# Performance work log

Measured on AMD Instinct MI355X. Metric: run time of the kernel, lower is better.

## Reference

```python
import jax, jax.numpy as jnp
import numpy as np

B, H, E, V = 128, 1024, 1024, 40000
L, S, A = 256, 10, 10
L_S, L_A = 1.0, 1.0  # s_copy_lambda / a_copy_lambda
NEG = -1e24


def setup_inputs():
    key = jax.random.key(0)
    ks = jax.random.split(key, 32)
    n = lambda i, shape: jax.random.normal(ks[i], shape, dtype=jnp.float32)
    p = lambda i, shape: jax.random.normal(ks[i], shape, dtype=jnp.float32) * 0.02
    rnn_in = 3 * E + H  # embed + history ctx (H) + state ctx (E) + action ctx (E)
    return {
        "inp": n(0, (B, 1, E)),
        "hidden": n(1, (1, B, H)),
        "hs_vectors": n(2, (B, L, H)),
        "state_gumbel_prob": jax.random.uniform(ks[3], (B, S, V), dtype=jnp.float32),
        "state_gumbel_embed": n(4, (B, S, E)),
        "action_gumbel_prob": jax.random.uniform(ks[5], (B, A, V), dtype=jnp.float32),
        "action_gumbel_embed": n(6, (B, A, E)),
        "history_lens": jax.random.randint(ks[7], (B,), 1, L + 1),
        "history_word_indices": jax.random.randint(ks[8], (B, L), 0, V),
        # history word mlp-attention
        "Wq_hist": p(9, (H, H)), "bq_hist": jnp.zeros((H,), jnp.float32),
        "Wm_hist": p(10, (H, H)), "v_hist": p(11, (H,)),
        # init_s_attn / init_a_attn (query H, memory E)
        "Wq_s": p(12, (H, H)), "bq_s": jnp.zeros((H,), jnp.float32),
        "Wm_s": p(13, (E, H)), "v_s": p(14, (H,)),
        "Wq_a": p(15, (H, H)), "bq_a": jnp.zeros((H,), jnp.float32),
        "Wm_a": p(16, (E, H)), "v_a": p(17, (H,)),
        # sparse_copy_attn (memory E+1)
        "Wq_sc": p(18, (H, H)), "bq_sc": jnp.zeros((H,), jnp.float32),
        "Wm_sc": p(19, (E + 1, H)), "v_sc": p(20, (H,)),
        # GRU (torch layout: [3H, in], gate order r,z,n)
        "W_ih": p(21, (3 * H, rnn_in)), "W_hh": p(22, (3 * H, H)),
        "b_ih": jnp.zeros((3 * H,), jnp.float32), "b_hh": jnp.zeros((3 * H,), jnp.float32),
        # output projection
        "W_out": p(23, (H, V)), "b_out": jnp.zeros((V,), jnp.float32),
    }


def _mlp_scores(q, mem, Wq, bq, Wm, v):
    # q: [B,1,H], mem: [B,L,M] -> additive-attention logits [B,1,L]
    t = jnp.tanh((q @ Wq + bq) + (mem @ Wm))  # [B,L,H]
    return (t @ v)[:, None, :]


def reference(inp, hidden, hs_vectors, state_gumbel_prob, state_gumbel_embed,
              action_gumbel_prob, action_gumbel_embed, history_lens,
              history_word_indices, Wq_hist, bq_hist, Wm_hist, v_hist,
              Wq_s, bq_s, Wm_s, v_s, Wq_a, bq_a, Wm_a, v_a,
              Wq_sc, bq_sc, Wm_sc, v_sc, W_ih, W_hh, b_ih, b_hh, W_out, b_out):
    q0 = jnp.transpose(hidden, (1, 0, 2))  # [B,1,H]
    # --- history word attention (masked mlp attention) ---
    hist_scores = _mlp_scores(q0, hs_vectors, Wq_hist, bq_hist, Wm_hist, v_hist)
    valid = jnp.arange(L)[None, None, :] < history_lens[:, None, None]
    hist_scores = jnp.where(valid, hist_scores, NEG)
    c_his = jax.nn.softmax(hist_scores, axis=-1) @ hs_vectors  # [B,1,H]
    # --- init_consult over state / action gumbel embeddings ---
    sw = jax.nn.softmax(_mlp_scores(q0, state_gumbel_embed, Wq_s, bq_s, Wm_s, v_s), axis=-1)
    c_state = sw @ state_gumbel_embed  # [B,1,E]
    aw = jax.nn.softmax(_mlp_scores(q0, action_gumbel_embed, Wq_a, bq_a, Wm_a, v_a), axis=-1)
    c_action = aw @ action_gumbel_embed  # [B,1,E]
    x = jnp.concatenate([inp, c_his, c_state, c_action], axis=-1)[:, 0, :]  # [B,3E+H]
    # --- single-step GRU cell (torch semantics, gate order r,z,n) ---
    h0 = hidden[0]
    gi = x @ W_ih.T + b_ih
    gh = h0 @ W_hh.T + b_hh
    ir, iz, inn = jnp.split(gi, 3, axis=-1)
    hr, hz, hn = jnp.split(gh, 3, axis=-1)
    r = jax.nn.sigmoid(ir + hr)
    z = jax.nn.sigmoid(iz + hz)
    nact = jnp.tanh(inn + r * hn)
    h_new = (1.0 - z) * nact + z * h0  # [B,H]
    # --- vocab logits + copy logits, joint softmax ---
    gene_logits = h_new @ W_out + b_out  # [B,V]
    cq = h_new[:, None, :]
    hs_logits = jnp.einsum('bqh,blh->bql', cq, hs_vectors)[:, 0, :]  # dot attn, [B,L]
    s_tag = jnp.zeros((B, S, 1), jnp.float32)
    a_tag = jnp.ones((B, A, 1), jnp.float32)
    st_logits = _mlp_scores(cq, jnp.concatenate([state_gumbel_embed, s_tag], -1), Wq_sc, bq_sc, Wm_sc, v_sc)[:, 0, :]
    ac_logits = _mlp_scores(cq, jnp.concatenate([action_gumbel_embed, a_tag], -1), Wq_sc, bq_sc, Wm_sc, v_sc)[:, 0, :]
    all_logits = jnp.concatenate([gene_logits, hs_logits, st_logits, ac_logits], axis=-1)
    wp = jax.nn.softmax(all_logits, axis=-1)  # [B, V+L+S+A]
    gene_p = wp[:, :V]
    hs_w = wp[:, V:V + L]
    st_w = wp[:, V + L:V + L + S]
    ac_w = wp[:, V + L + S:]
    # --- copy-distribution mixing ---
    scp = jnp.einsum('bs,bsv->bv', st_w, state_gumbel_prob)
    acp = jnp.einsum('ba,bav->bv', ac_w, action_gumbel_prob)
    gene_p = gene_p + L_S * scp + L_A * acp
    copy_p = jnp.zeros((B, V), jnp.float32).at[jnp.arange(B)[:, None], history_word_indices].add(hs_w)
    out = jnp.log(gene_p + copy_p)[:, None, :]  # [B,1,V]
    return out, h_new[None]
```

## Files before the change

### kernel.cpp

```cpp
#include <hip/hip_runtime.h>
#include <stdint.h>

typedef __attribute__((ext_vector_type(4))) float f32x4;
typedef __attribute__((ext_vector_type(2))) unsigned int u32x2;
typedef __attribute__((ext_vector_type(4))) unsigned int u32x4;
typedef __attribute__((ext_vector_type(8))) short bf16x8;

#define BV (128*40000)

__device__ __forceinline__ unsigned rne_bf16(float f) {
    unsigned x = __float_as_uint(f);
    return ((x + 0x7FFFu + ((x >> 16) & 1u)) >> 16) & 0xFFFFu;
}
__device__ __forceinline__ unsigned pack2(float a, float b) {
    return rne_bf16(a) | (rne_bf16(b) << 16);
}
__device__ __forceinline__ float bf2f(unsigned u) {
    return __uint_as_float((u & 0xFFFFu) << 16);
}
__device__ __forceinline__ float sigm(float x) { return 1.0f / (1.0f + expf(-x)); }
__device__ __forceinline__ float ftanh(float x) {
    float e = __expf(2.0f * x);
    return 1.0f - 2.0f / (e + 1.0f);
}

__device__ __forceinline__ void gload16(const void* g, void* l) {
    __builtin_amdgcn_global_load_lds(
        (const __attribute__((address_space(1))) unsigned*)g,
        (__attribute__((address_space(3))) unsigned*)l, 16, 0, 0);
}

struct BigArgs {
    const unsigned short *hs, *WmhT, *se, *ae, *WmsT, *WmaT, *WmscT;
    const float *qh_h, *bq_h, *v_h;
    const float *qh_s, *bq_s, *v_s;
    const float *qh_a, *bq_a, *v_a;
    float *hsc, *stsc, *acsc;
    unsigned short *mseh, *maeh;
};

__global__ __launch_bounds__(512, 1) void k_big(
    BigArgs a, int* __restrict__ ctr, const int* __restrict__ prefix,
    const int* __restrict__ ntp) {
    __shared__ unsigned short As[2][16384];
    __shared__ unsigned short Bs[2][16384];
    __shared__ int sTile;
    __shared__ int rows_tab[256];

    const int nTiles = ntp[0], Mp = ntp[1];
    const int t = threadIdx.x, lane = t & 63, wv = t >> 6;
    const int l16 = lane & 15, lq = lane >> 4;
    const int wm = wv >> 2, wn = wv & 3;
    const int srowL = t >> 3;
    const int gccA = ((t & 7) ^ (srowL & 7)) << 3;
    const int swz = l16 & 7;
    const int c0 = ((lq ^ swz) << 3);
    const int A0 = (wm << 13) + (l16 << 6);
    const int B0 = ((wn >> 1) << 13) + ((((wn & 1) << 6) + l16) << 6);

#define STQA(ktt, d, q) gload16(gAr[q] + (ktt) * 64, &As[d][((q) << 12) + (wv << 9)])
#define STQB(ktt, d, q) gload16(gB + ((size_t)(q) << 16) + (ktt) * 64, &Bs[d][((q) << 12) + (wv << 9)])

    for (;;) {
        __syncthreads();
        if (t == 0) sTile = atomicAdd(ctr, 1);
        __syncthreads();
        const int wg = sTile;
        if (wg >= nTiles) return;

        const unsigned short *Abase, *Bt;
        const float *rb = nullptr, *cb = nullptr, *vv = nullptr;
        float* out = nullptr;
        unsigned short* outh = nullptr;
        int m0, n0, vrows, cls;
        if (wg < 40) {
            cls = 0;
            int op = wg / 20, r = wg - op * 20;
            int mt = r >> 2, nt2 = r & 3;
            if (op == 0) { Abase = a.se; Bt = a.WmsT; rb = a.qh_s; cb = a.bq_s; vv = a.v_s; out = a.stsc; }
            else         { Abase = a.ae; Bt = a.WmaT; rb = a.qh_a; cb = a.bq_a; vv = a.v_a; out = a.acsc; }
            m0 = mt << 8; n0 = nt2 << 8; vrows = 256;
        } else if (wg < 80) {
            cls = 1;
            int r = wg - 40;
            int op = r / 20; r -= op * 20;
            int mt = r >> 2, nt2 = r & 3;
            Abase = op ? a.ae : a.se; Bt = a.WmscT;
            outh = op ? a.maeh : a.mseh;
            m0 = mt << 8; n0 = nt2 << 8; vrows = 256;
        } else {
            cls = 2;
            int h = wg - 80;
            int m = h >> 2, n = h & 3;
            Abase = a.hs; Bt = a.WmhT; rb = a.qh_h; cb = a.bq_h; vv = a.v_h; out = a.hsc;
            m0 = m << 8; n0 = n << 8;
            vrows = Mp - m0; if (vrows > 256) vrows = 256;
        }

        if (t < 256) {
            int rid;
            if (cls != 2) {
                rid = m0 + t;
            } else {
                int g = m0 + t;
                if (g < Mp) {
                    int lo = 0, hi = 128;
                    while (hi - lo > 1) {
                        int mid = (lo + hi) >> 1;
                        if (prefix[mid] <= g) lo = mid; else hi = mid;
                    }
                    rid = (lo << 8) + (g - prefix[lo]);
                } else {
                    rid = 0;
                }
            }
            rows_tab[t] = rid;
        }
        __syncthreads();

        const unsigned short* gAr[4];
#pragma unroll
        for (int q = 0; q < 4; ++q)
            gAr[q] = Abase + ((size_t)rows_tab[srowL + (q << 6)] << 10) + gccA;
        const unsigned short* gB = Bt + (size_t)(n0 + srowL) * 1024 + gccA;

        f32x4 acc[8][4];
#pragma unroll
        for (int i = 0; i < 8; ++i)
#pragma unroll
            for (int j = 0; j < 4; ++j) acc[i][j] = (f32x4){0.f, 0.f, 0.f, 0.f};

        STQA(0, 0, 0); STQA(0, 0, 2);
        STQB(0, 0, 0); STQB(0, 0, 1); STQB(0, 0, 2); STQB(0, 0, 3);
        STQA(0, 0, 1); STQA(0, 0, 3);
        __builtin_amdgcn_sched_barrier(0);
        asm volatile("s_waitcnt vmcnt(2)" ::: "memory");
        __builtin_amdgcn_s_barrier();
        __builtin_amdgcn_sched_barrier(0);

        for (int kt = 0; kt < 16; ++kt) {
            const int cur = kt & 1, dn = cur ^ 1, kn = kt + 1;
            const bool pre = kt < 15;
            const unsigned short* ab = As[cur];
            const unsigned short* bb = Bs[cur];
            bf16x8 bk0[4], bk1[4], af[4];
            if (pre) { STQA(kn, dn, 0); STQA(kn, dn, 2); }
#pragma unroll
            for (int nf = 0; nf < 4; ++nf) bk0[nf] = *(const bf16x8*)(bb + B0 + (nf << 10) + c0);
#pragma unroll
            for (int mf = 0; mf < 4; ++mf) af[mf] = *(const bf16x8*)(ab + A0 + (mf << 10) + c0);
            __builtin_amdgcn_s_setprio(1);
#pragma unroll
            for (int mf = 0; mf < 4; ++mf)
#pragma unroll
                for (int nf = 0; nf < 4; ++nf)
                    acc[mf][nf] = __builtin_amdgcn_mfma_f32_16x16x32_bf16(af[mf], bk0[nf], acc[mf][nf], 0, 0, 0);
            __builtin_amdgcn_s_setprio(0);
            if (pre) { STQB(kn, dn, 0); STQB(kn, dn, 1); }
#pragma unroll
            for (int nf = 0; nf < 4; ++nf) bk1[nf] = *(const bf16x8*)(bb + B0 + (nf << 10) + (c0 ^ 32));
#pragma unroll
            for (int mf = 0; mf < 4; ++mf) af[mf] = *(const bf16x8*)(ab + A0 + (mf << 10) + (c0 ^ 32));
            __builtin_amdgcn_s_setprio(1);
#pragma unroll
            for (int mf = 0; mf < 4; ++mf)
#pragma unroll
                for (int nf = 0; nf < 4; ++nf)
                    acc[mf][nf] = __builtin_amdgcn_mfma_f32_16x16x32_bf16(af[mf], bk1[nf], acc[mf][nf], 0, 0, 0);
            __builtin_amdgcn_s_setprio(0);
            if (pre) { STQB(kn, dn, 2); STQB(kn, dn, 3); }
            __builtin_amdgcn_sched_barrier(0);
            if (pre) asm volatile("s_waitcnt vmcnt(6)" ::: "memory");
            else     asm volatile("s_waitcnt vmcnt(0)" ::: "memory");
            __builtin_amdgcn_s_barrier();
            __builtin_amdgcn_sched_barrier(0);
#pragma unroll
            for (int mf = 0; mf < 4; ++mf) af[mf] = *(const bf16x8*)(ab + A0 + ((4 + mf) << 10) + c0);
            __builtin_amdgcn_s_setprio(1);
#pragma unroll
            for (int mf = 0; mf < 4; ++mf)
#pragma unroll
                for (int nf = 0; nf < 4; ++nf)
                    acc[4 + mf][nf] = __builtin_amdgcn_mfma_f32_16x16x32_bf16(af[mf], bk0[nf], acc[4 + mf][nf], 0, 0, 0);
            __builtin_amdgcn_s_setprio(0);
            if (pre) { STQA(kn, dn, 1); STQA(kn, dn, 3); }
#pragma unroll
            for (int mf = 0; mf < 4; ++mf) af[mf] = *(const bf16x8*)(ab + A0 + ((4 + mf) << 10) + (c0 ^ 32));
            __builtin_amdgcn_s_setprio(1);
#pragma unroll
            for (int mf = 0; mf < 4; ++mf)
#pragma unroll
                for (int nf = 0; nf < 4; ++nf)
                    acc[4 + mf][nf] = __builtin_amdgcn_mfma_f32_16x16x32_bf16(af[mf], bk1[nf], acc[4 + mf][nf], 0, 0, 0);
            __builtin_amdgcn_s_setprio(0);
            __builtin_amdgcn_sched_barrier(0);
            if (pre) asm volatile("s_waitcnt vmcnt(2)" ::: "memory");
            else     asm volatile("s_waitcnt vmcnt(0)" ::: "memory");
            __builtin_amdgcn_s_barrier();
            __builtin_amdgcn_sched_barrier(0);
        }

        if (cls == 1) {
            int gcs4[4];
#pragma unroll
            for (int nf = 0; nf < 4; ++nf) gcs4[nf] = n0 + (wn << 6) + (nf << 4) + l16;
#pragma unroll
            for (int mf = 0; mf < 8; ++mf) {
#pragma unroll
                for (int r = 0; r < 4; ++r) {
                    int grow = m0 + (wm << 7) + (mf << 4) + (lq << 2) + r;
#pragma unroll
                    for (int nf = 0; nf < 4; ++nf)
                        outh[(size_t)grow * 1024 + gcs4[nf]] = (unsigned short)rne_bf16(acc[mf][nf][r]);
                }
            }
        } else {
            float cbv[4], vvv[4];
            int gcs[4];
#pragma unroll
            for (int nf = 0; nf < 4; ++nf) {
                int gc = n0 + (wn << 6) + (nf << 4) + l16;
                gcs[nf] = gc; cbv[nf] = cb[gc]; vvv[nf] = vv[gc];
            }
#pragma unroll
            for (int mf = 0; mf < 8; ++mf) {
                int rloc = (wm << 7) + (mf << 4);
                if (rloc < vrows) {
#pragma unroll
                    for (int r = 0; r < 4; ++r) {
                        int lrow = rloc + (lq << 2) + r;
                        if (lrow >= vrows) continue;
                        int gr = m0 + lrow;
                        int bidx = (cls == 2) ? (rows_tab[lrow] >> 8) : (gr / 10);
                        const float* rbp = rb + ((size_t)bidx << 10);
                        float s = 0.f;
#pragma unroll
                        for (int nf = 0; nf < 4; ++nf) {
                            float x = acc[mf][nf][r] + rbp[gcs[nf]] + cbv[nf];
                            s += ftanh(x) * vvv[nf];
                        }
#pragma unroll
                        for (int m2 = 1; m2 < 16; m2 <<= 1) s += __shfl_xor(s, m2, 64);
                        if (l16 == 0) atomicAdd(&out[gr], s);
                    }
                }
            }
        }
    }
#undef STQA
#undef STQB
}

__device__ __forceinline__ void mgemm2(
    const unsigned short* __restrict__ A, const unsigned short* __restrict__ Bt,
    float* __restrict__ out,
    int m0, int n0, int kb, int ke, int ldk, int ldc)
{
    __shared__ unsigned short As[2][4096];
    __shared__ unsigned short Bs[2][4096];
    const int t = threadIdx.x, lane = t & 63, wv = t >> 6;
    const int l16 = lane & 15, lq = lane >> 4;
    const int wm = wv >> 1, wn = wv & 1;

    const int srow = lane >> 2, scol = (lane & 3) << 3;
    const unsigned short* gA0 = A + (size_t)(m0 + (wv << 4) + srow) * ldk + kb + scol;
    const unsigned short* gA1 = gA0 + (size_t)64 * ldk;
    const unsigned short* gB0 = Bt + (size_t)(n0 + (wv << 4) + srow) * ldk + kb + scol;
    const unsigned short* gB1 = gB0 + (size_t)64 * ldk;
    unsigned short* lA0 = &As[0][wv << 9];
    unsigned short* lA1 = &As[0][(wv + 4) << 9];
    unsigned short* lB0 = &Bs[0][wv << 9];
    unsigned short* lB1 = &Bs[0][(wv + 4) << 9];

    f32x4 acc[4][4];
#pragma unroll
    for (int i = 0; i < 4; ++i)
#pragma unroll
        for (int j = 0; j < 4; ++j) acc[i][j] = (f32x4){0.f, 0.f, 0.f, 0.f};

    const int NS = (ke - kb) >> 5;
    gload16(gA0, lA0); gload16(gA1, lA1);
    gload16(gB0, lB0); gload16(gB1, lB1);

    for (int s = 0; s < NS; ++s) {
        __syncthreads();
        if (s + 1 < NS) {
            const int nb = (s + 1) & 1, ko = (s + 1) << 5;
            gload16(gA0 + ko, lA0 + (nb << 12)); gload16(gA1 + ko, lA1 + (nb << 12));
            gload16(gB0 + ko, lB0 + (nb << 12)); gload16(gB1 + ko, lB1 + (nb << 12));
        }
        const unsigned short* ab = As[s & 1];
        const unsigned short* bb = Bs[s & 1];
        bf16x8 af[4], bfv[4];
#pragma unroll
        for (int i = 0; i < 4; ++i)
            af[i] = *(const bf16x8*)(ab + (((wm << 6) + (i << 4) + l16) << 5) + (lq << 3));
#pragma unroll
        for (int i = 0; i < 4; ++i)
            bfv[i] = *(const bf16x8*)(bb + (((wn << 6) + (i << 4) + l16) << 5) + (lq << 3));
#pragma unroll
        for (int mf = 0; mf < 4; ++mf)
#pragma unroll
            for (int nf = 0; nf < 4; ++nf)
                acc[mf][nf] = __builtin_amdgcn_mfma_f32_16x16x32_bf16(af[mf], bfv[nf], acc[mf][nf], 0, 0, 0);
    }

#pragma unroll
    for (int mf = 0; mf < 4; ++mf) {
        int gr0 = m0 + (wm << 6) + (mf << 4) + (lq << 2);
#pragma unroll
        for (int nf = 0; nf < 4; ++nf) {
            int gc = n0 + (wn << 6) + (nf << 4) + l16;
#pragma unroll
            for (int r = 0; r < 4; ++r)
                atomicAdd(&out[(size_t)(gr0 + r) * ldc + gc], acc[mf][nf][r]);
        }
    }
}

__device__ __forceinline__ void gene_body(
    const unsigned short* __restrict__ hnb, const float* __restrict__ Wout,
    const float* __restrict__ b_out, float* __restrict__ out, int n0)
{
    __shared__ unsigned short As[2][4096];
    __shared__ unsigned short Bs[2][4096];
    const int t = threadIdx.x, lane = t & 63, wv = t >> 6;
    const int l16 = lane & 15, lq = lane >> 4;
    const int wm = wv >> 1, wn = wv & 1;

    const int srow = lane >> 2, scol = (lane & 3) << 3;
    const unsigned short* gA0 = hnb + (size_t)((wv << 4) + srow) * 1024 + scol;
    const unsigned short* gA1 = gA0 + (size_t)64 * 1024;
    unsigned short* lA0 = &As[0][wv << 9];
    unsigned short* lA1 = &As[0][(wv + 4) << 9];

    const int bn = t & 127, kh = t >> 7;
    const bool ok = (n0 + bn) < 40000;
    const float* gB = Wout + (size_t)(kh * 16) * 40000 + (n0 + bn);

    f32x4 acc[4][4];
#pragma unroll
    for (int i = 0; i < 4; ++i)
#pragma unroll
        for (int j = 0; j < 4; ++j) acc[i][j] = (f32x4){0.f, 0.f, 0.f, 0.f};

    auto stageB = [&](int buf, int ko) {
        const float* src = gB + (size_t)ko * 40000;
        float f[16];
#pragma unroll
        for (int j = 0; j < 16; ++j) f[j] = ok ? src[(size_t)j * 40000] : 0.0f;
        u32x4* d = (u32x4*)&Bs[buf][bn * 32 + kh * 16];
        d[0] = (u32x4){pack2(f[0],f[1]), pack2(f[2],f[3]), pack2(f[4],f[5]), pack2(f[6],f[7])};
        d[1] = (u32x4){pack2(f[8],f[9]), pack2(f[10],f[11]), pack2(f[12],f[13]), pack2(f[14],f[15])};
    };

    gload16(gA0, lA0); gload16(gA1, lA1); stageB(0, 0);
    for (int s = 0; s < 32; ++s) {
        __syncthreads();
        if (s + 1 < 32) {
            const int nb = (s + 1) & 1, ko = (s + 1) << 5;
            gload16(gA0 + ko, lA0 + (nb << 12)); gload16(gA1 + ko, lA1 + (nb << 12));
            stageB(nb, ko);
        }
        const unsigned short* ab = As[s & 1];
        const unsigned short* bb = Bs[s & 1];
        bf16x8 af[4], bfv[4];
#pragma unroll
        for (int i = 0; i < 4; ++i)
            af[i] = *(const bf16x8*)(ab + (((wm << 6) + (i << 4) + l16) << 5) + (lq << 3));
#pragma unroll
        for (int i = 0; i < 4; ++i)
            bfv[i] = *(const bf16x8*)(bb + (((wn << 6) + (i << 4) + l16) << 5) + (lq << 3));
#pragma unroll
        for (int mf = 0; mf < 4; ++mf)
#pragma unroll
            for (int nf = 0; nf < 4; ++nf)
                acc[mf][nf] = __builtin_amdgcn_mfma_f32_16x16x32_bf16(af[mf], bfv[nf], acc[mf][nf], 0, 0, 0);
    }
#pragma unroll
    for (int mf = 0; mf < 4; ++mf) {
        int gr0 = (wm << 6) + (mf << 4) + (lq << 2);
#pragma unroll
        for (int nf = 0; nf < 4; ++nf) {
            int gc = n0 + (wn << 6) + (nf << 4) + l16;
            if (gc < 40000) {
                float bo = b_out[gc];
#pragma unroll
                for (int r = 0; r < 4; ++r)
                    out[(size_t)(gr0 + r) * 40000 + gc] = acc[mf][nf][r] + bo;
            }
        }
    }
}

__global__ __launch_bounds__(256) void k_qh4(
    const unsigned short* q0, const unsigned short* W0, const unsigned short* W1,
    const unsigned short* W2, float* o0, float* o1, float* o2) {
    const unsigned short* W = W0; float* o = o0;
    if (blockIdx.z == 1) { W = W1; o = o1; }
    if (blockIdx.z == 2) { W = W2; o = o2; }
    int kb = blockIdx.y << 8;
    mgemm2(q0, W, o, 0, blockIdx.x * 128, kb, kb + 256, 1024, 1024);
}

__global__ __launch_bounds__(256) void k_gigh2(
    const unsigned short* xb, const unsigned short* q0,
    const unsigned short* Wih, const unsigned short* Whh, float* gi, float* gh) {
    if (blockIdx.z == 0) {
        int kb = blockIdx.y << 9;
        mgemm2(xb, Wih, gi, 0, blockIdx.x * 128, kb, kb + 512, 4096, 3072);
    } else {
        if (blockIdx.y >= 2) return;
        int kb = blockIdx.y << 9;
        mgemm2(q0, Whh, gh, 0, blockIdx.x * 128, kb, kb + 512, 1024, 3072);
    }
}

__global__ __launch_bounds__(256) void k_geneR(
    const unsigned short* __restrict__ hnb, const float* __restrict__ Wout,
    const float* __restrict__ b_out, float* __restrict__ out,
    const float* __restrict__ sprob, const float* __restrict__ aprob,
    const float* __restrict__ wtil, float* __restrict__ R) {
    int id = blockIdx.x;
    if (id < 313) {
        gene_body(hnb, Wout, b_out, out, id << 7);
        return;
    }
    int rid = id - 313;
    int b = rid / 40, ch = rid - b * 40;
    int t = threadIdx.x;
    __shared__ float wsb[20];
    if (t < 20) wsb[t] = wtil[b * 20 + t];
    __syncthreads();
    if (t >= 250) return;
    int v4 = ch * 250 + t;
    size_t base = (size_t)b * 10000 + v4;
    f32x4 r = {0.f, 0.f, 0.f, 0.f};
#pragma unroll
    for (int s = 0; s < 10; ++s) {
        f32x4 pv = ((const f32x4*)sprob)[((size_t)b * 10 + s) * 10000 + v4];
        f32x4 av = ((const f32x4*)aprob)[((size_t)b * 10 + s) * 10000 + v4];
        float ws = wsb[s], wa = wsb[10 + s];
#pragma unroll
        for (int j = 0; j < 4; ++j) r[j] += ws * pv[j] + wa * av[j];
    }
    ((f32x4*)R)[base] = r;
}

struct PrepArgs {
    const float* cs[6]; unsigned short* cd[6]; int pre[7];
    const float* ts[8]; unsigned short* td[8];
    const int* lens; int* prefix; int* nt;
};
__global__ __launch_bounds__(256) void k_prep(PrepArgs a) {
    int bid = blockIdx.x, t = threadIdx.x;
    if (bid < 2048) {
        __shared__ float tile[64][65];
        int z = bid >> 8, rem = bid & 255, y = rem >> 4, x = rem & 15;
        const float* in = a.ts[z];
        unsigned short* ot = a.td[z];
        int k0 = y << 6, n0 = x << 6;
        int tr = t >> 6, tc = t & 63;
#pragma unroll
        for (int i = 0; i < 16; ++i) {
            int r = (i << 2) + tr;
            tile[r][tc] = in[(size_t)(k0 + r) * 1024 + n0 + tc];
        }
        __syncthreads();
#pragma unroll
        for (int i = 0; i < 16; ++i) {
            int r = (i << 2) + tr;
            ot[(size_t)(n0 + r) * 1024 + k0 + tc] = (unsigned short)rne_bf16(tile[tc][r]);
        }
    } else if (bid == 2048) {
        __shared__ int sc[128];
        if (t < 128) sc[t] = a.lens[t];
        __syncthreads();
        for (int off = 1; off < 128; off <<= 1) {
            int x = (t >= off && t < 128) ? sc[t - off] : 0;
            __syncthreads();
            if (t < 128) sc[t] += x;
            __syncthreads();
        }
        if (t == 0) a.prefix[0] = 0;
        if (t < 128) a.prefix[t + 1] = sc[t];
        if (t == 127) {
            int Mp = sc[127];
            a.nt[0] = 80 + (((Mp + 255) >> 8) << 2);
            a.nt[1] = Mp;
        }
    } else {
        int total = a.pre[6];
        for (int i = (bid - 2049) * 256 + t; i < total; i += 2048 * 256) {
            int seg = 0;
            while (i >= a.pre[seg + 1]) ++seg;
            int loc = i - a.pre[seg];
            const f32x4* s4 = (const f32x4*)a.cs[seg] + (size_t)loc * 2;
            f32x4 q0 = s4[0], q1 = s4[1];
            ((u32x4*)a.cd[seg])[loc] =
                (u32x4){pack2(q0[0],q0[1]), pack2(q0[2],q0[3]), pack2(q1[0],q1[1]), pack2(q1[2],q1[3])};
        }
    }
}

__device__ __forceinline__ void softmax10(const float* src, float* dst) {
    float m = src[0];
    for (int i = 1; i < 10; ++i) m = fmaxf(m, src[i]);
    float z = 0.f, e[10];
    for (int i = 0; i < 10; ++i) { e[i] = expf(src[i] - m); z += e[i]; }
    float iz = 1.0f / z;
    for (int i = 0; i < 10; ++i) dst[i] = e[i] * iz;
}

__global__ __launch_bounds__(256) void k_ctx(
    const float* __restrict__ scores, const int* __restrict__ lens,
    const int* __restrict__ prefix,
    const unsigned short* __restrict__ hs,
    const float* __restrict__ inp, const float* __restrict__ st_sc, const float* __restrict__ ac_sc,
    const unsigned short* __restrict__ se, const unsigned short* __restrict__ ae,
    unsigned short* __restrict__ xb) {
    int b = blockIdx.x, t = threadIdx.x;
    __shared__ float w[256];
    __shared__ float red[256];
    __shared__ float sw[10], aw[10];
    int len = lens[b];
    int base = prefix[b];
    bool valid = t < len;
    float s = valid ? scores[base + t] : -3.0e38f;
    red[t] = s;
    __syncthreads();
    for (int st = 128; st > 0; st >>= 1) { if (t < st) red[t] = fmaxf(red[t], red[t + st]); __syncthreads(); }
    float m = red[0];
    __syncthreads();
    float e = valid ? expf(s - m) : 0.0f;
    red[t] = e;
    __syncthreads();
    for (int st = 128; st > 0; st >>= 1) { if (t < st) red[t] += red[t + st]; __syncthreads(); }
    float Z = red[0];
    __syncthreads();
    w[t] = e / Z;
    if (t == 0) softmax10(st_sc + b * 10, sw);
    if (t == 64) softmax10(ac_sc + b * 10, aw);
    f32x4 iv = ((const f32x4*)(inp + (size_t)b * 1024))[t];
    *((u32x2*)(xb + (size_t)b * 4096) + t) = (u32x2){pack2(iv[0], iv[1]), pack2(iv[2], iv[3])};
    __syncthreads();
    float a0 = 0.f, a1 = 0.f, a2 = 0.f, a3 = 0.f;
    for (int l = 0; l < 256; ++l) {
        float wl = w[l];
        if (wl == 0.0f) continue;
        u32x2 u = *((const u32x2*)(hs + ((size_t)b * 256 + l) * 1024) + t);
        a0 += wl * bf2f(u[0]); a1 += wl * bf2f(u[0] >> 16);
        a2 += wl * bf2f(u[1]); a3 += wl * bf2f(u[1] >> 16);
    }
    *((u32x2*)(xb + (size_t)b * 4096 + 1024) + t) = (u32x2){pack2(a0, a1), pack2(a2, a3)};
    float cs0=0,cs1=0,cs2=0,cs3=0, ca0=0,ca1=0,ca2=0,ca3=0;
#pragma unroll
    for (int q = 0; q < 10; ++q) {
        u32x2 us = *((const u32x2*)(se + ((size_t)b * 10 + q) * 1024) + t);
        u32x2 ua = *((const u32x2*)(ae + ((size_t)b * 10 + q) * 1024) + t);
        float ws = sw[q], wa = aw[q];
        cs0 += ws * bf2f(us[0]); cs1 += ws * bf2f(us[0] >> 16);
        cs2 += ws * bf2f(us[1]); cs3 += ws * bf2f(us[1] >> 16);
        ca0 += wa * bf2f(ua[0]); ca1 += wa * bf2f(ua[0] >> 16);
        ca2 += wa * bf2f(ua[1]); ca3 += wa * bf2f(ua[1] >> 16);
    }
    *((u32x2*)(xb + (size_t)b * 4096 + 2048) + t) = (u32x2){pack2(cs0, cs1), pack2(cs2, cs3)};
    *((u32x2*)(xb + (size_t)b * 4096 + 3072) + t) = (u32x2){pack2(ca0, ca1), pack2(ca2, ca3)};
}

__global__ __launch_bounds__(1024) void k_gruhsl(
    const float* __restrict__ gi, const float* __restrict__ gh,
    const float* __restrict__ b_ih, const float* __restrict__ b_hh,
    const float* __restrict__ h0, float* __restrict__ hnew,
    unsigned short* __restrict__ hnb,
    const unsigned short* __restrict__ hs, float* __restrict__ hsl,
    const unsigned short* __restrict__ WqscT, float* __restrict__ qsc) {
    int b = blockIdx.x, y = blockIdx.y, j = threadIdx.x;
    size_t i = (size_t)b * 1024 + j;
    const float* gib = gi + (size_t)b * 3072;
    const float* ghb = gh + (size_t)b * 3072;
    float r = sigm(gib[j] + b_ih[j] + ghb[j] + b_hh[j]);
    float z = sigm(gib[1024 + j] + b_ih[1024 + j] + ghb[1024 + j] + b_hh[1024 + j]);
    float hn = ghb[2048 + j] + b_hh[2048 + j];
    float n = tanhf(gib[2048 + j] + b_ih[2048 + j] + r * hn);
    float h = (1.0f - z) * n + z * h0[i];
    if (y == 0) {
        hnew[i] = h;
        hnb[i] = (unsigned short)rne_bf16(h);
    }
    __shared__ float hsm[1024];
    hsm[j] = h;
    __syncthreads();
    {
        float acn = 0.f;
        const u32x4* wr = (const u32x4*)(WqscT + ((size_t)j << 10));
        int st = y << 6;
#pragma unroll 4
        for (int k8 = st; k8 < st + 64; ++k8) {
            u32x4 u = wr[k8];
            const float* hp = hsm + (k8 << 3);
            acn += hp[0]*bf2f(u[0]) + hp[1]*bf2f(u[0]>>16)
                 + hp[2]*bf2f(u[1]) + hp[3]*bf2f(u[1]>>16)
                 + hp[4]*bf2f(u[2]) + hp[5]*bf2f(u[2]>>16)
                 + hp[6]*bf2f(u[3]) + hp[7]*bf2f(u[3]>>16);
        }
        atomicAdd(&qsc[(size_t)b * 1024 + j], acn);
    }
    int wave = j >> 6, lane = j & 63;
    float hr[16];
#pragma unroll
    for (int k = 0; k < 16; ++k) hr[k] = hsm[lane * 16 + k];
    for (int l = (y << 7) + wave; l < (y << 7) + 128; l += 16) {
        const u32x4* row = (const u32x4*)(hs + ((size_t)b * 256 + l) * 1024);
        u32x4 u0 = row[lane * 2], u1 = row[lane * 2 + 1];
        float s = hr[0]*bf2f(u0[0]) + hr[1]*bf2f(u0[0]>>16) + hr[2]*bf2f(u0[1]) + hr[3]*bf2f(u0[1]>>16)
                + hr[4]*bf2f(u0[2]) + hr[5]*bf2f(u0[2]>>16) + hr[6]*bf2f(u0[3]) + hr[7]*bf2f(u0[3]>>16)
                + hr[8]*bf2f(u1[0]) + hr[9]*bf2f(u1[0]>>16) + hr[10]*bf2f(u1[1]) + hr[11]*bf2f(u1[1]>>16)
                + hr[12]*bf2f(u1[2]) + hr[13]*bf2f(u1[2]>>16) + hr[14]*bf2f(u1[3]) + hr[15]*bf2f(u1[3]>>16);
#pragma unroll
        for (int msk = 1; msk < 64; msk <<= 1) s += __shfl_xor(s, msk, 64);
        if (lane == 0) hsl[b * 256 + l] = s;
    }
}

__global__ __launch_bounds__(256) void k_stacep(
    const unsigned short* __restrict__ mseh, const unsigned short* __restrict__ maeh,
    const float* __restrict__ qsc, const float* __restrict__ bq_sc,
    const float* __restrict__ v_sc, const float* __restrict__ tagrow,
    float* __restrict__ stlg, float* __restrict__ aclg,
    float* __restrict__ mtil, float* __restrict__ wtil) {
    int b = blockIdx.x, t = threadIdx.x, w = t >> 6, lane = t & 63;
    __shared__ float res[20];
    const float* qb = qsc + (size_t)b * 1024;
    for (int r = w; r < 20; r += 4) {
        bool ac = r >= 10;
        int s = ac ? r - 10 : r;
        const unsigned short* mm = (ac ? maeh : mseh) + ((size_t)b * 10 + s) * 1024;
        float acc = 0.f;
#pragma unroll
        for (int j2 = 0; j2 < 16; ++j2) {
            int c = lane + (j2 << 6);
            float x = bf2f(mm[c]) + qb[c] + bq_sc[c];
            if (ac) x += tagrow[c];
            acc += ftanh(x) * v_sc[c];
        }
#pragma unroll
        for (int m2 = 1; m2 < 64; m2 <<= 1) acc += __shfl_xor(acc, m2, 64);
        if (lane == 0) res[r] = acc;
    }
    __syncthreads();
    if (t < 10) stlg[b * 10 + t] = res[t];
    if (t >= 64 && t < 74) aclg[b * 10 + (t - 64)] = res[10 + (t - 64)];
    if (t == 128) {
        float mt = res[0];
        for (int i2 = 1; i2 < 20; ++i2) mt = fmaxf(mt, res[i2]);
        mtil[b] = mt;
        for (int i2 = 0; i2 < 20; ++i2) wtil[b * 20 + i2] = expf(res[i2] - mt);
    }
}

__global__ __launch_bounds__(256) void k_smsc(
    const float* __restrict__ gene, const float* __restrict__ hsl,
    const float* __restrict__ stl, const float* __restrict__ acl,
    const int* __restrict__ hwi,
    float* __restrict__ mbuf, float* __restrict__ zbuf, float* __restrict__ copyp) {
    int b = blockIdx.x, t = threadIdx.x;
    __shared__ float red[256];
    const f32x4* g4 = (const f32x4*)(gene + (size_t)b * 40000);
    float mx = -3.0e38f;
    for (int i = t; i < 10000; i += 256) {
        f32x4 q = g4[i];
        mx = fmaxf(mx, fmaxf(fmaxf(q[0], q[1]), fmaxf(q[2], q[3])));
    }
    float hv = hsl[b * 256 + t];
    mx = fmaxf(mx, hv);
    if (t < 10) mx = fmaxf(mx, fmaxf(stl[b * 10 + t], acl[b * 10 + t]));
    red[t] = mx; __syncthreads();
    for (int s = 128; s > 0; s >>= 1) { if (t < s) red[t] = fmaxf(red[t], red[t + s]); __syncthreads(); }
    float m = red[0];
    __syncthreads();
    float sum = 0.f;
    for (int i = t; i < 10000; i += 256) {
        f32x4 q = g4[i];
        sum += expf(q[0]-m) + expf(q[1]-m) + expf(q[2]-m) + expf(q[3]-m);
    }
    sum += expf(hv - m);
    if (t < 10) sum += expf(stl[b * 10 + t] - m) + expf(acl[b * 10 + t] - m);
    red[t] = sum; __syncthreads();
    for (int s = 128; s > 0; s >>= 1) { if (t < s) red[t] += red[t + s]; __syncthreads(); }
    float Z = red[0];
    if (t == 0) { mbuf[b] = m; zbuf[b] = Z; }
    float wv = expf(hv - m) / Z;
    atomicAdd(copyp + (size_t)b * 40000 + hwi[b * 256 + t], wv);
}

__global__ __launch_bounds__(256) void k_final(
    float* __restrict__ gene_out, const float* __restrict__ copyp,
    const float* __restrict__ R, const float* __restrict__ mbuf,
    const float* __restrict__ zbuf, const float* __restrict__ mtil) {
    int b = blockIdx.y, t = threadIdx.x;
    int v4 = blockIdx.x * 256 + t;
    if (v4 < 10000) {
        float m = mbuf[b], iz = 1.0f / zbuf[b];
        float sb = expf(mtil[b] - m) * iz;
        size_t base = (size_t)b * 10000 + v4;
        f32x4 g = ((const f32x4*)gene_out)[base];
        f32x4 c = ((const f32x4*)copyp)[base];
        f32x4 rr = ((const f32x4*)R)[base];
        f32x4 r;
#pragma unroll
        for (int j = 0; j < 4; ++j)
            r[j] = logf(expf(g[j] - m) * iz + c[j] + rr[j] * sb);
        ((f32x4*)gene_out)[base] = r;
    }
}

#define OFF_QH_H  0
#define OFF_QH_S  131072
#define OFF_QH_A  262144
#define OFF_QSC   393216
#define OFF_GI    524288
#define OFF_GH    917504
#define OFF_HSC   1310720
#define OFF_STSC  1343488
#define OFF_ACSC  1344768
#define OFF_STLG  1346048
#define OFF_ACLG  1347328
#define OFF_CTR   1348608
#define OFF_PFX   1348736
#define OFF_NT    1348904
#define ZERO_FLOATS 1348936
#define OFF_HSL   1348992
#define OFF_M     1381760
#define OFF_Z     1381888
#define OFF_COPY  1382016
#define OFF_MTIL  6502016
#define OFF_WTIL  6502144
#define FLOAT_TOTAL 6504704
#define SO_HS     0
#define SO_SE     33554432
#define SO_AE     34865152
#define SO_Q0     36175872
#define SO_X      36306944
#define SO_HNB    36831232
#define SO_WQHT   36962304
#define SO_WQST   38010880
#define SO_WQAT   39059456
#define SO_WQSCT  40108032
#define SO_WMHT   41156608
#define SO_WMST   42205184
#define SO_WMAT   43253760
#define SO_WMSCT  44302336
#define SO_WIH    45350912
#define SO_WHH    57933824
#define SO_MSE    61079552
#define SO_MAE    62390272

extern "C" void kernel_launch(void* const* d_in, const int* in_sizes, int n_in,
                              void* d_out, int out_size, void* d_ws, size_t ws_size,
                              hipStream_t stream) {
    const float* inp     = (const float*)d_in[0];
    const float* hidden  = (const float*)d_in[1];
    const float* hs      = (const float*)d_in[2];
    const float* sprob   = (const float*)d_in[3];
    const float* se      = (const float*)d_in[4];
    const float* aprob   = (const float*)d_in[5];
    const float* ae      = (const float*)d_in[6];
    const int*   lens    = (const int*)d_in[7];
    const int*   hwi     = (const int*)d_in[8];
    const float* Wq_hist = (const float*)d_in[9];
    const float* bq_hist = (const float*)d_in[10];
    const float* Wm_hist = (const float*)d_in[11];
    const float* v_hist  = (const float*)d_in[12];
    const float* Wq_s    = (const float*)d_in[13];
    const float* bq_s    = (const float*)d_in[14];
    const float* Wm_s    = (const float*)d_in[15];
    const float* v_s     = (const float*)d_in[16];
    const float* Wq_a    = (const float*)d_in[17];
    const float* bq_a    = (const float*)d_in[18];
    const float* Wm_a    = (const float*)d_in[19];
    const float* v_a     = (const float*)d_in[20];
    const float* Wq_sc   = (const float*)d_in[21];
    const float* bq_sc   = (const float*)d_in[22];
    const float* Wm_sc   = (const float*)d_in[23];
    const float* v_sc    = (const float*)d_in[24];
    const float* W_ih    = (const float*)d_in[25];
    const float* W_hh    = (const float*)d_in[26];
    const float* b_ih    = (const float*)d_in[27];
    const float* b_hh    = (const float*)d_in[28];
    const float* W_out   = (const float*)d_in[29];
    const float* b_out   = (const float*)d_in[30];

    float* out  = (float*)d_out;
    float* w    = (float*)d_ws;
    float* hnew = out + BV;
    unsigned short* sb = (unsigned short*)(w + FLOAT_TOTAL);

    float* qh_h = w + OFF_QH_H;  float* qh_s = w + OFF_QH_S;  float* qh_a = w + OFF_QH_A;
    float* qsc  = w + OFF_QSC;   float* gi   = w + OFF_GI;    float* gh   = w + OFF_GH;
    float* hsc  = w + OFF_HSC;   float* stsc = w + OFF_STSC;  float* acsc = w + OFF_ACSC;
    float* stlg = w + OFF_STLG;  float* aclg = w + OFF_ACLG;
    float* hsl  = w + OFF_HSL;   float* mbuf = w + OFF_M;     float* zbuf = w + OFF_Z;
    float* copyp = w + OFF_COPY;
    float* mtil = w + OFF_MTIL;  float* wtil = w + OFF_WTIL;
    int*   ctr  = (int*)(w + OFF_CTR);
    int*   pfx  = (int*)(w + OFF_PFX);
    int*   ntb  = (int*)(w + OFF_NT);

    unsigned short* hs_bf = sb + SO_HS;   unsigned short* se_bf = sb + SO_SE;
    unsigned short* ae_bf = sb + SO_AE;   unsigned short* q0_bf = sb + SO_Q0;
    unsigned short* x_bf  = sb + SO_X;    unsigned short* hnb   = sb + SO_HNB;
    unsigned short* WqhT  = sb + SO_WQHT; unsigned short* WqsT  = sb + SO_WQST;
    unsigned short* WqaT  = sb + SO_WQAT; unsigned short* WqscT = sb + SO_WQSCT;
    unsigned short* WmhT  = sb + SO_WMHT; unsigned short* WmsT  = sb + SO_WMST;
    unsigned short* WmaT  = sb + SO_WMAT; unsigned short* WmscT = sb + SO_WMSCT;
    unsigned short* WihB  = sb + SO_WIH;  unsigned short* WhhB  = sb + SO_WHH;
    unsigned short* mseh  = sb + SO_MSE;  unsigned short* maeh  = sb + SO_MAE;
    float* Rbuf = (float*)(sb + SO_WIH);

    dim3 blk(256);

    hipMemsetAsync(w, 0, (size_t)ZERO_FLOATS * 4, stream);
    hipMemsetAsync(copyp, 0, (size_t)BV * 4, stream);

    PrepArgs pa;
    pa.cs[0]=hs; pa.cs[1]=se; pa.cs[2]=ae; pa.cs[3]=hidden; pa.cs[4]=W_ih; pa.cs[5]=W_hh;
    pa.cd[0]=hs_bf; pa.cd[1]=se_bf; pa.cd[2]=ae_bf; pa.cd[3]=q0_bf; pa.cd[4]=WihB; pa.cd[5]=WhhB;
    pa.pre[0]=0; pa.pre[1]=4194304; pa.pre[2]=4358144; pa.pre[3]=4521984;
    pa.pre[4]=4538368; pa.pre[5]=6111232; pa.pre[6]=6504448;
    pa.ts[0]=Wq_hist; pa.ts[1]=Wq_s; pa.ts[2]=Wq_a; pa.ts[3]=Wq_sc;
    pa.ts[4]=Wm_hist; pa.ts[5]=Wm_s; pa.ts[6]=Wm_a; pa.ts[7]=Wm_sc;
    pa.td[0]=WqhT; pa.td[1]=WqsT; pa.td[2]=WqaT; pa.td[3]=WqscT;
    pa.td[4]=WmhT; pa.td[5]=WmsT; pa.td[6]=WmaT; pa.td[7]=WmscT;
    pa.lens = lens; pa.prefix = pfx; pa.nt = ntb;
    k_prep<<<dim3(4097), blk, 0, stream>>>(pa);

    k_qh4<<<dim3(8, 4, 3), blk, 0, stream>>>(q0_bf, WqhT, WqsT, WqaT, qh_h, qh_s, qh_a);

    BigArgs ba;
    ba.hs = hs_bf; ba.WmhT = WmhT; ba.se = se_bf; ba.ae = ae_bf;
    ba.WmsT = WmsT; ba.WmaT = WmaT; ba.WmscT = WmscT;
    ba.qh_h = qh_h; ba.bq_h = bq_hist; ba.v_h = v_hist;
    ba.qh_s = qh_s; ba.bq_s = bq_s; ba.v_s = v_s;
    ba.qh_a = qh_a; ba.bq_a = bq_a; ba.v_a = v_a;
    ba.hsc = hsc; ba.stsc = stsc; ba.acsc = acsc;
    ba.mseh = mseh; ba.maeh = maeh;
    k_big<<<dim3(256), dim3(512), 0, stream>>>(ba, ctr, pfx, ntb);

    k_ctx<<<dim3(128), blk, 0, stream>>>(hsc, lens, pfx, hs_bf, inp, stsc, acsc, se_bf, ae_bf, x_bf);
    k_gigh2<<<dim3(24, 8, 2), blk, 0, stream>>>(x_bf, q0_bf, WihB, WhhB, gi, gh);
    k_gruhsl<<<dim3(128, 2), dim3(1024), 0, stream>>>(gi, gh, b_ih, b_hh, hidden, hnew, hnb,
                                                      hs_bf, hsl, WqscT, qsc);
    k_stacep<<<dim3(128), blk, 0, stream>>>(mseh, maeh, qsc, bq_sc, v_sc,
                                            Wm_sc + (size_t)1024 * 1024, stlg, aclg, mtil, wtil);
    k_geneR<<<dim3(313 + 5120), blk, 0, stream>>>(hnb, W_out, b_out, out, sprob, aprob, wtil, Rbuf);
    k_smsc<<<dim3(128), blk, 0, stream>>>(out, hsl, stlg, aclg, hwi, mbuf, zbuf, copyp);
    k_final<<<dim3(40, 128), blk, 0, stream>>>(out, copyp, Rbuf, mbuf, zbuf, mtil);

    (void)in_sizes; (void)n_in; (void)out_size; (void)ws_size;
}
```

Before: 561.6 us.

## Fold query projections, GRU weight conversion and sparse-copy scoring into existing kernels

Moves the three query-projection GEMMs into k_big as its first persistent tiles, with other tiles spin-waiting on a completion counter. The W_ih/W_hh bf16 conversion moves from k_prep into trailing k_big tiles. The k_stacep kernel is folded into k_gruhsl, and k_geneR now computes the exp weights itself. Some sched_barriers in the GEMM loop are also removed. This removes kernel launches and serial gaps, at the cost of a cross-block spin dependency and a single-block-column qsc computation in the GRU kernel.

```diff
diff --git a/kernel.cpp b/kernel.cpp
--- a/kernel.cpp
+++ b/kernel.cpp
@@ -32,22 +32,24 @@
 
 struct BigArgs {
     const unsigned short *hs, *WmhT, *se, *ae, *WmsT, *WmaT, *WmscT;
-    const float *qh_h, *bq_h, *v_h;
-    const float *qh_s, *bq_s, *v_s;
-    const float *qh_a, *bq_a, *v_a;
+    const unsigned short *q0, *Wq0T, *Wq1T, *Wq2T;
+    const float *Wihf, *Whhf;
+    unsigned short *WihB, *WhhB;
+    const float *bq_h, *v_h, *bq_s, *v_s, *bq_a, *v_a;
+    float *qh_h, *qh_s, *qh_a;
     float *hsc, *stsc, *acsc;
     unsigned short *mseh, *maeh;
 };
 
 __global__ __launch_bounds__(512, 1) void k_big(
-    BigArgs a, int* __restrict__ ctr, const int* __restrict__ prefix,
-    const int* __restrict__ ntp) {
+    BigArgs a, int* __restrict__ ctr, int* __restrict__ dqh,
+    const int* __restrict__ prefix, const int* __restrict__ ntp) {
     __shared__ unsigned short As[2][16384];
     __shared__ unsigned short Bs[2][16384];
     __shared__ int sTile;
     __shared__ int rows_tab[256];
 
-    const int nTiles = ntp[0], Mp = ntp[1];
+    const int nTiles = ntp[0], Mp = ntp[1], cvtb = ntp[2];
     const int t = threadIdx.x, lane = t & 63, wv = t >> 6;
     const int l16 = lane & 15, lq = lane >> 4;
     const int wm = wv >> 2, wn = wv & 3;
@@ -68,21 +70,44 @@
         const int wg = sTile;
         if (wg >= nTiles) return;
 
+        if (wg >= cvtb) {
+            const int G_IH = 1572864;
+            int g0 = (wg - cvtb) * 30720 + t;
+#pragma unroll 4
+            for (int it = 0; it < 60; ++it, g0 += 512) {
+                const f32x4* s4;
+                u32x4* d4;
+                if (g0 < G_IH) { s4 = (const f32x4*)a.Wihf + (size_t)g0 * 2; d4 = (u32x4*)a.WihB + g0; }
+                else { int g2 = g0 - G_IH; s4 = (const f32x4*)a.Whhf + (size_t)g2 * 2; d4 = (u32x4*)a.WhhB + g2; }
+                f32x4 q0 = s4[0], q1 = s4[1];
+                *d4 = (u32x4){pack2(q0[0],q0[1]), pack2(q0[2],q0[3]), pack2(q1[0],q1[1]), pack2(q1[2],q1[3])};
+            }
+            continue;
+        }
+
         const unsigned short *Abase, *Bt;
         const float *rb = nullptr, *cb = nullptr, *vv = nullptr;
         float* out = nullptr;
         unsigned short* outh = nullptr;
         int m0, n0, vrows, cls;
-        if (wg < 40) {
+        if (wg < 12) {
+            cls = 4;
+            int op = wg >> 2;
+            Abase = a.q0;
+            Bt = (op == 0) ? a.Wq0T : (op == 1) ? a.Wq1T : a.Wq2T;
+            out = (op == 0) ? a.qh_h : (op == 1) ? a.qh_s : a.qh_a;
+            m0 = 0; n0 = (wg & 3) << 8; vrows = 128;
+        } else if (wg < 52) {
             cls = 0;
-            int op = wg / 20, r = wg - op * 20;
+            int r = wg - 12;
+            int op = r / 20; r -= op * 20;
             int mt = r >> 2, nt2 = r & 3;
             if (op == 0) { Abase = a.se; Bt = a.WmsT; rb = a.qh_s; cb = a.bq_s; vv = a.v_s; out = a.stsc; }
             else         { Abase = a.ae; Bt = a.WmaT; rb = a.qh_a; cb = a.bq_a; vv = a.v_a; out = a.acsc; }
             m0 = mt << 8; n0 = nt2 << 8; vrows = 256;
-        } else if (wg < 80) {
+        } else if (wg < 92) {
             cls = 1;
-            int r = wg - 40;
+            int r = wg - 52;
             int op = r / 20; r -= op * 20;
             int mt = r >> 2, nt2 = r & 3;
             Abase = op ? a.ae : a.se; Bt = a.WmscT;
@@ -90,7 +115,7 @@
             m0 = mt << 8; n0 = nt2 << 8; vrows = 256;
         } else {
             cls = 2;
-            int h = wg - 80;
+            int h = wg - 92;
             int m = h >> 2, n = h & 3;
             Abase = a.hs; Bt = a.WmhT; rb = a.qh_h; cb = a.bq_h; vv = a.v_h; out = a.hsc;
             m0 = m << 8; n0 = n << 8;
@@ -136,7 +161,6 @@
         __builtin_amdgcn_sched_barrier(0);
         asm volatile("s_waitcnt vmcnt(2)" ::: "memory");
         __builtin_amdgcn_s_barrier();
-        __builtin_amdgcn_sched_barrier(0);
 
         for (int kt = 0; kt < 16; ++kt) {
             const int cur = kt & 1, dn = cur ^ 1, kn = kt + 1;
@@ -173,7 +197,6 @@
             if (pre) asm volatile("s_waitcnt vmcnt(6)" ::: "memory");
             else     asm volatile("s_waitcnt vmcnt(0)" ::: "memory");
             __builtin_amdgcn_s_barrier();
-            __builtin_amdgcn_sched_barrier(0);
 #pragma unroll
             for (int mf = 0; mf < 4; ++mf) af[mf] = *(const bf16x8*)(ab + A0 + ((4 + mf) << 10) + c0);
             __builtin_amdgcn_s_setprio(1);
@@ -197,7 +220,6 @@
             if (pre) asm volatile("s_waitcnt vmcnt(2)" ::: "memory");
             else     asm volatile("s_waitcnt vmcnt(0)" ::: "memory");
             __builtin_amdgcn_s_barrier();
-            __builtin_amdgcn_sched_barrier(0);
         }
 
         if (cls == 1) {
@@ -214,7 +236,28 @@
                         outh[(size_t)grow * 1024 + gcs4[nf]] = (unsigned short)rne_bf16(acc[mf][nf][r]);
                 }
             }
+        } else if (cls == 4) {
+#pragma unroll
+            for (int mf = 0; mf < 8; ++mf) {
+                int rloc = (wm << 7) + (mf << 4);
+                if (rloc < vrows) {
+#pragma unroll
+                    for (int r = 0; r < 4; ++r) {
+                        int gr = rloc + (lq << 2) + r;
+#pragma unroll
+                        for (int nf = 0; nf < 4; ++nf) {
+                            int gc = n0 + (wn << 6) + (nf << 4) + l16;
+                            out[(size_t)gr * 1024 + gc] = acc[mf][nf][r];
+                        }
+                    }
+                }
+            }
+            __threadfence();
+            __syncthreads();
+            if (t == 0) atomicAdd(dqh, 1);
         } else {
+            if (t == 0) { while (atomicAdd(dqh, 0) < 12) { } }
+            __syncthreads();
             float cbv[4], vvv[4];
             int gcs[4];
 #pragma unroll
@@ -393,16 +436,6 @@
     }
 }
 
-__global__ __launch_bounds__(256) void k_qh4(
-    const unsigned short* q0, const unsigned short* W0, const unsigned short* W1,
-    const unsigned short* W2, float* o0, float* o1, float* o2) {
-    const unsigned short* W = W0; float* o = o0;
-    if (blockIdx.z == 1) { W = W1; o = o1; }
-    if (blockIdx.z == 2) { W = W2; o = o2; }
-    int kb = blockIdx.y << 8;
-    mgemm2(q0, W, o, 0, blockIdx.x * 128, kb, kb + 256, 1024, 1024);
-}
-
 __global__ __launch_bounds__(256) void k_gigh2(
     const unsigned short* xb, const unsigned short* q0,
     const unsigned short* Wih, const unsigned short* Whh, float* gi, float* gh) {
@@ -420,7 +453,8 @@
     const unsigned short* __restrict__ hnb, const float* __restrict__ Wout,
     const float* __restrict__ b_out, float* __restrict__ out,
     const float* __restrict__ sprob, const float* __restrict__ aprob,
-    const float* __restrict__ wtil, float* __restrict__ R) {
+    const float* __restrict__ stlg, const float* __restrict__ aclg,
+    const float* __restrict__ mtil, float* __restrict__ R) {
     int id = blockIdx.x;
     if (id < 313) {
         gene_body(hnb, Wout, b_out, out, id << 7);
@@ -430,7 +464,8 @@
     int b = rid / 40, ch = rid - b * 40;
     int t = threadIdx.x;
     __shared__ float wsb[20];
-    if (t < 20) wsb[t] = wtil[b * 20 + t];
+    if (t < 10) wsb[t] = expf(stlg[b * 10 + t] - mtil[b]);
+    else if (t < 20) wsb[t] = expf(aclg[b * 10 + (t - 10)] - mtil[b]);
     __syncthreads();
     if (t >= 250) return;
     int v4 = ch * 250 + t;
@@ -448,7 +483,7 @@
 }
 
 struct PrepArgs {
-    const float* cs[6]; unsigned short* cd[6]; int pre[7];
+    const float* cs[4]; unsigned short* cd[4]; int pre[5];
     const float* ts[8]; unsigned short* td[8];
     const int* lens; int* prefix; int* nt;
 };
@@ -486,11 +521,13 @@
         if (t < 128) a.prefix[t + 1] = sc[t];
         if (t == 127) {
             int Mp = sc[127];
-            a.nt[0] = 80 + (((Mp + 255) >> 8) << 2);
+            int H4 = ((Mp + 255) >> 8) << 2;
+            a.nt[0] = 92 + H4 + 64;
             a.nt[1] = Mp;
+            a.nt[2] = 92 + H4;
         }
     } else {
-        int total = a.pre[6];
+        int total = a.pre[4];
         for (int i = (bid - 2049) * 256 + t; i < total; i += 2048 * 256) {
             int seg = 0;
             while (i >= a.pre[seg + 1]) ++seg;
@@ -574,7 +611,11 @@
     const float* __restrict__ h0, float* __restrict__ hnew,
     unsigned short* __restrict__ hnb,
     const unsigned short* __restrict__ hs, float* __restrict__ hsl,
-    const unsigned short* __restrict__ WqscT, float* __restrict__ qsc) {
+    const unsigned short* __restrict__ WqscT,
+    const unsigned short* __restrict__ mseh, const unsigned short* __restrict__ maeh,
+    const float* __restrict__ bq_sc, const float* __restrict__ v_sc,
+    const float* __restrict__ tagrow,
+    float* __restrict__ stlg, float* __restrict__ aclg, float* __restrict__ mtil) {
     int b = blockIdx.x, y = blockIdx.y, j = threadIdx.x;
     size_t i = (size_t)b * 1024 + j;
     const float* gib = gi + (size_t)b * 3072;
@@ -584,19 +625,20 @@
     float hn = ghb[2048 + j] + b_hh[2048 + j];
     float n = tanhf(gib[2048 + j] + b_ih[2048 + j] + r * hn);
     float h = (1.0f - z) * n + z * h0[i];
+    __shared__ float hsm[1024];
+    __shared__ float qs[1024];
+    __shared__ float res[20];
     if (y == 0) {
         hnew[i] = h;
         hnb[i] = (unsigned short)rne_bf16(h);
     }
-    __shared__ float hsm[1024];
     hsm[j] = h;
     __syncthreads();
-    {
+    if (y == 0) {
         float acn = 0.f;
         const u32x4* wr = (const u32x4*)(WqscT + ((size_t)j << 10));
-        int st = y << 6;
 #pragma unroll 4
-        for (int k8 = st; k8 < st + 64; ++k8) {
+        for (int k8 = 0; k8 < 128; ++k8) {
             u32x4 u = wr[k8];
             const float* hp = hsm + (k8 << 3);
             acn += hp[0]*bf2f(u[0]) + hp[1]*bf2f(u[0]>>16)
@@ -604,9 +646,38 @@
                  + hp[4]*bf2f(u[2]) + hp[5]*bf2f(u[2]>>16)
                  + hp[6]*bf2f(u[3]) + hp[7]*bf2f(u[3]>>16);
         }
-        atomicAdd(&qsc[(size_t)b * 1024 + j], acn);
-    }
+        qs[j] = acn + bq_sc[j];
+    }
+    __syncthreads();
     int wave = j >> 6, lane = j & 63;
+    if (y == 0) {
+        for (int rr = wave; rr < 20; rr += 16) {
+            bool ac = rr >= 10;
+            int s5 = ac ? rr - 10 : rr;
+            const unsigned short* mm = (ac ? maeh : mseh) + ((size_t)b * 10 + s5) * 1024;
+            float acc2 = 0.f;
+#pragma unroll
+            for (int k2 = 0; k2 < 16; ++k2) {
+                int c = lane + (k2 << 6);
+                float x = bf2f(mm[c]) + qs[c];
+                if (ac) x += tagrow[c];
+                acc2 += ftanh(x) * v_sc[c];
+            }
+#pragma unroll
+            for (int m2 = 1; m2 < 64; m2 <<= 1) acc2 += __shfl_xor(acc2, m2, 64);
+            if (lane == 0) res[rr] = acc2;
+        }
+    }
+    __syncthreads();
+    if (y == 0) {
+        if (j < 10) stlg[b * 10 + j] = res[j];
+        if (j >= 64 && j < 74) aclg[b * 10 + (j - 64)] = res[10 + (j - 64)];
+        if (j == 128) {
+            float mt = res[0];
+            for (int i2 = 1; i2 < 20; ++i2) mt = fmaxf(mt, res[i2]);
+            mtil[b] = mt;
+        }
+    }
     float hr[16];
 #pragma unroll
     for (int k = 0; k < 16; ++k) hr[k] = hsm[lane * 16 + k];
@@ -620,42 +691,6 @@
 #pragma unroll
         for (int msk = 1; msk < 64; msk <<= 1) s += __shfl_xor(s, msk, 64);
         if (lane == 0) hsl[b * 256 + l] = s;
-    }
-}
-
-__global__ __launch_bounds__(256) void k_stacep(
-    const unsigned short* __restrict__ mseh, const unsigned short* __restrict__ maeh,
-    const float* __restrict__ qsc, const float* __restrict__ bq_sc,
-    const float* __restrict__ v_sc, const float* __restrict__ tagrow,
-    float* __restrict__ stlg, float* __restrict__ aclg,
-    float* __restrict__ mtil, float* __restrict__ wtil) {
-    int b = blockIdx.x, t = threadIdx.x, w = t >> 6, lane = t & 63;
-    __shared__ float res[20];
-    const float* qb = qsc + (size_t)b * 1024;
-    for (int r = w; r < 20; r += 4) {
-        bool ac = r >= 10;
-        int s = ac ? r - 10 : r;
-        const unsigned short* mm = (ac ? maeh : mseh) + ((size_t)b * 10 + s) * 1024;
-        float acc = 0.f;
-#pragma unroll
-        for (int j2 = 0; j2 < 16; ++j2) {
-            int c = lane + (j2 << 6);
-            float x = bf2f(mm[c]) + qb[c] + bq_sc[c];
-            if (ac) x += tagrow[c];
-            acc += ftanh(x) * v_sc[c];
-        }
-#pragma unroll
-        for (int m2 = 1; m2 < 64; m2 <<= 1) acc += __shfl_xor(acc, m2, 64);
-        if (lane == 0) res[r] = acc;
-    }
-    __syncthreads();
-    if (t < 10) stlg[b * 10 + t] = res[t];
-    if (t >= 64 && t < 74) aclg[b * 10 + (t - 64)] = res[10 + (t - 64)];
-    if (t == 128) {
-        float mt = res[0];
-        for (int i2 = 1; i2 < 20; ++i2) mt = fmaxf(mt, res[i2]);
-        mtil[b] = mt;
-        for (int i2 = 0; i2 < 20; ++i2) wtil[b * 20 + i2] = expf(res[i2] - mt);
     }
 }
 
@@ -727,6 +762,7 @@
 #define OFF_STLG  1346048
 #define OFF_ACLG  1347328
 #define OFF_CTR   1348608
+#define OFF_DQH   1348610
 #define OFF_PFX   1348736
 #define OFF_NT    1348904
 #define ZERO_FLOATS 1348936
@@ -735,7 +771,6 @@
 #define OFF_Z     1381888
 #define OFF_COPY  1382016
 #define OFF_MTIL  6502016
-#define OFF_WTIL  6502144
 #define FLOAT_TOTAL 6504704
 #define SO_HS     0
 #define SO_SE     33554432
@@ -797,13 +832,14 @@
     unsigned short* sb = (unsigned short*)(w + FLOAT_TOTAL);
 
     float* qh_h = w + OFF_QH_H;  float* qh_s = w + OFF_QH_S;  float* qh_a = w + OFF_QH_A;
-    float* qsc  = w + OFF_QSC;   float* gi   = w + OFF_GI;    float* gh   = w + OFF_GH;
+    float* gi   = w + OFF_GI;    float* gh   = w + OFF_GH;
     float* hsc  = w + OFF_HSC;   float* stsc = w + OFF_STSC;  float* acsc = w + OFF_ACSC;
     float* stlg = w + OFF_STLG;  float* aclg = w + OFF_ACLG;
     float* hsl  = w + OFF_HSL;   float* mbuf = w + OFF_M;     float* zbuf = w + OFF_Z;
     float* copyp = w + OFF_COPY;
-    float* mtil = w + OFF_MTIL;  float* wtil = w + OFF_WTIL;
+    float* mtil = w + OFF_MTIL;
     int*   ctr  = (int*)(w + OFF_CTR);
+    int*   dqh  = (int*)(w + OFF_DQH);
     int*   pfx  = (int*)(w + OFF_PFX);
     int*   ntb  = (int*)(w + OFF_NT);
 
@@ -824,10 +860,9 @@
     hipMemsetAsync(copyp, 0, (size_t)BV * 4, stream);
 
     PrepArgs pa;
-    pa.cs[0]=hs; pa.cs[1]=se; pa.cs[2]=ae; pa.cs[3]=hidden; pa.cs[4]=W_ih; pa.cs[5]=W_hh;
-    pa.cd[0]=hs_bf; pa.cd[1]=se_bf; pa.cd[2]=ae_bf; pa.cd[3]=q0_bf; pa.cd[4]=WihB; pa.cd[5]=WhhB;
-    pa.pre[0]=0; pa.pre[1]=4194304; pa.pre[2]=4358144; pa.pre[3]=4521984;
-    pa.pre[4]=4538368; pa.pre[5]=6111232; pa.pre[6]=6504448;
+    pa.cs[0]=hs; pa.cs[1]=se; pa.cs[2]=ae; pa.cs[3]=hidden;
+    pa.cd[0]=hs_bf; pa.cd[1]=se_bf; pa.cd[2]=ae_bf; pa.cd[3]=q0_bf;
+    pa.pre[0]=0; pa.pre[1]=4194304; pa.pre[2]=4358144; pa.pre[3]=4521984; pa.pre[4]=4538368;
     pa.ts[0]=Wq_hist; pa.ts[1]=Wq_s; pa.ts[2]=Wq_a; pa.ts[3]=Wq_sc;
     pa.ts[4]=Wm_hist; pa.ts[5]=Wm_s; pa.ts[6]=Wm_a; pa.ts[7]=Wm_sc;
     pa.td[0]=WqhT; pa.td[1]=WqsT; pa.td[2]=WqaT; pa.td[3]=WqscT;
@@ -835,25 +870,26 @@
     pa.lens = lens; pa.prefix = pfx; pa.nt = ntb;
     k_prep<<<dim3(4097), blk, 0, stream>>>(pa);
 
-    k_qh4<<<dim3(8, 4, 3), blk, 0, stream>>>(q0_bf, WqhT, WqsT, WqaT, qh_h, qh_s, qh_a);
-
     BigArgs ba;
     ba.hs = hs_bf; ba.WmhT = WmhT; ba.se = se_bf; ba.ae = ae_bf;
     ba.WmsT = WmsT; ba.WmaT = WmaT; ba.WmscT = WmscT;
-    ba.qh_h = qh_h; ba.bq_h = bq_hist; ba.v_h = v_hist;
-    ba.qh_s = qh_s; ba.bq_s = bq_s; ba.v_s = v_s;
-    ba.qh_a = qh_a; ba.bq_a = bq_a; ba.v_a = v_a;
+    ba.q0 = q0_bf; ba.Wq0T = WqhT; ba.Wq1T = WqsT; ba.Wq2T = WqaT;
+    ba.Wihf = W_ih; ba.Whhf = W_hh; ba.WihB = WihB; ba.WhhB = WhhB;
+    ba.bq_h = bq_hist; ba.v_h = v_hist;
+    ba.bq_s = bq_s; ba.v_s = v_s;
+    ba.bq_a = bq_a; ba.v_a = v_a;
+    ba.qh_h = qh_h; ba.qh_s = qh_s; ba.qh_a = qh_a;
     ba.hsc = hsc; ba.stsc = stsc; ba.acsc = acsc;
     ba.mseh = mseh; ba.maeh = maeh;
-    k_big<<<dim3(256), dim3(512), 0, stream>>>(ba, ctr, pfx, ntb);
+    k_big<<<dim3(256), dim3(512), 0, stream>>>(ba, ctr, dqh, pfx, ntb);
 
     k_ctx<<<dim3(128), blk, 0, stream>>>(hsc, lens, pfx, hs_bf, inp, stsc, acsc, se_bf, ae_bf, x_bf);
     k_gigh2<<<dim3(24, 8, 2), blk, 0, stream>>>(x_bf, q0_bf, WihB, WhhB, gi, gh);
     k_gruhsl<<<dim3(128, 2), dim3(1024), 0, stream>>>(gi, gh, b_ih, b_hh, hidden, hnew, hnb,
-                                                      hs_bf, hsl, WqscT, qsc);
-    k_stacep<<<dim3(128), blk, 0, stream>>>(mseh, maeh, qsc, bq_sc, v_sc,
-                                            Wm_sc + (size_t)1024 * 1024, stlg, aclg, mtil, wtil);
-    k_geneR<<<dim3(313 + 5120), blk, 0, stream>>>(hnb, W_out, b_out, out, sprob, aprob, wtil, Rbuf);
+                                                      hs_bf, hsl, WqscT, mseh, maeh, bq_sc, v_sc,
+                                                      Wm_sc + (size_t)1024 * 1024, stlg, aclg, mtil);
+    k_geneR<<<dim3(313 + 5120), blk, 0, stream>>>(hnb, W_out, b_out, out, sprob, aprob,
+                                                  stlg, aclg, mtil, Rbuf);
     k_smsc<<<dim3(128), blk, 0, stream>>>(out, hsl, stlg, aclg, hwi, mbuf, zbuf, copyp);
     k_final<<<dim3(40, 128), blk, 0, stream>>>(out, copyp, Rbuf, mbuf, zbuf, mtil);
 
```

Result: slower. 573.8 us (+2.2%).
